# Optimization experiments

Hardware: AMD Instinct MI355X
Metric: run time of the kernel (lower is better)

## Reference

```python
import jax, jax.numpy as jnp
import numpy as np

VOCAB, EMB, HID = 50000, 1024, 2048
BATCH, SEQ = 256, 128


def _lstm_cell(x, h, c, W_ih, W_hh, b_ih, b_hh):
    # PyTorch LSTMCell: gates ordered (i, f, g, o), each of width HID
    gates = x @ W_ih.T + b_ih + h @ W_hh.T + b_hh  # [B, 4H]
    i, f, g, o = jnp.split(gates, 4, axis=-1)
    c_new = jax.nn.sigmoid(f) * c + jax.nn.sigmoid(i) * jnp.tanh(g)
    h_new = jax.nn.sigmoid(o) * jnp.tanh(c_new)
    return h_new, c_new


def setup_inputs() -> dict:
    key = jax.random.key(0)
    ks = jax.random.split(key, 11)
    s_e = 1.0 / np.sqrt(EMB)
    s_h = 1.0 / np.sqrt(HID)
    return {
        "inputs": jax.random.randint(ks[0], (BATCH, SEQ), 0, VOCAB, dtype=jnp.int64)
        if jax.config.jax_enable_x64 else jax.random.randint(ks[0], (BATCH, SEQ), 0, VOCAB, dtype=jnp.int32),
        "embed_table": jax.random.normal(ks[1], (VOCAB, EMB), jnp.float32),
        "W_ih_f": jax.random.normal(ks[2], (4 * HID, EMB), jnp.float32) * s_e,
        "W_hh_f": jax.random.normal(ks[3], (4 * HID, HID), jnp.float32) * s_h,
        "b_ih_f": jax.random.normal(ks[4], (4 * HID,), jnp.float32) * s_h,
        "b_hh_f": jax.random.normal(ks[5], (4 * HID,), jnp.float32) * s_h,
        "W_ih_b": jax.random.normal(ks[6], (4 * HID, EMB), jnp.float32) * s_e,
        "W_hh_b": jax.random.normal(ks[7], (4 * HID, HID), jnp.float32) * s_h,
        "b_ih_b": jax.random.normal(ks[8], (4 * HID,), jnp.float32) * s_h,
        "b_hh_b": jax.random.normal(ks[9], (4 * HID,), jnp.float32) * s_h,
    }


def reference(inputs, embed_table, W_ih_f, W_hh_f, b_ih_f, b_hh_f,
              W_ih_b, W_hh_b, b_ih_b, b_hh_b):
    # inputs[inputs > vocab_size] = 0
    idx = jnp.where(inputs > VOCAB, 0, inputs)
    embeds = embed_table[idx]  # [B, S, E]
    B = embeds.shape[0]
    zeros = jnp.zeros((B, HID), embeds.dtype)

    # Original forward loop feeds the (never-updated, all-zero) backward states
    # and discards cell state, so only the LAST timestep determines h_forward.
    h_fwd, _ = _lstm_cell(embeds[:, -1], zeros, zeros, W_ih_f, W_hh_f, b_ih_f, b_hh_f)

    # Backward loop: h recurses (t = S-1 .. 0), cell state stays zero (it is discarded).
    xs = jnp.flip(embeds, axis=1).transpose(1, 0, 2)  # [S, B, E], time-major reversed

    def step(h, x_t):
        h_new, _ = _lstm_cell(x_t, h, zeros, W_ih_b, W_hh_b, b_ih_b, b_hh_b)
        return h_new, None

    h_bwd, _ = jax.lax.scan(step, zeros, xs)

    return jnp.concatenate([h_fwd, h_bwd], axis=1)  # [B, 2H]
```

## Files before the change

kernel.cpp:

```cpp
#include <hip/hip_runtime.h>


#define B_    256
#define S_    128
#define E_    1024
#define H_    2048
#define VOC_  50000

typedef __bf16 bf16;
typedef bf16  bf16x8 __attribute__((ext_vector_type(8)));
typedef float f32x4  __attribute__((ext_vector_type(4)));
typedef float f32x16 __attribute__((ext_vector_type(16)));

typedef const char __attribute__((address_space(1)))* gas1_t;
typedef char       __attribute__((address_space(3)))* las3_t;

__global__ __launch_bounds__(256) void pack_w(const float* __restrict__ W,
                                              char* __restrict__ dst, int nchunks) {
  int p = blockIdx.x * 256 + threadIdx.x;
  int lane = p & 63; p >>= 6;
  int kk   = p & 3;  p >>= 2;
  int g    = p % 3;  p /= 3;
  int hl   = p & 1;  p >>= 1;
  int c    = p % nchunks;
  int jstrip = p / nchunks;
  int K  = nchunks * 64;
  int j  = jstrip * 32 + (lane & 31);
  int k0 = c * 64 + kk * 16 + (lane >> 5) * 8;
  int grow = j + (g == 1 ? 4096 : (g == 2 ? 6144 : 0));
  const float* src = W + (size_t)grow * K + k0;
  f32x4 v0 = *(const f32x4*)src;
  f32x4 v1 = *(const f32x4*)(src + 4);
  float f[8] = {v0[0], v0[1], v0[2], v0[3], v1[0], v1[1], v1[2], v1[3]};
  bf16x8 o;
#pragma unroll
  for (int e = 0; e < 8; ++e) {
    float x = f[e];
    bf16 hb = (bf16)x;
    o[e] = hl ? (bf16)(x - (float)hb) : hb;
  }
  size_t off = (size_t)(jstrip * nchunks + c) * 24576
             + (size_t)((hl * 3 + g) * 4 + kk) * 1024 + lane * 16;
  *(bf16x8*)(dst + off) = o;
}

__global__ __launch_bounds__(256) void pack_bias(const float* __restrict__ bib,
                                                 const float* __restrict__ bhb,
                                                 const float* __restrict__ bif,
                                                 const float* __restrict__ bhf,
                                                 float* __restrict__ B3B,
                                                 float* __restrict__ B3F) {
  int t = blockIdx.x * 256 + threadIdx.x;
  int which = t / 6144;
  int r = t % 6144;
  int g = r >> 11, j = r & 2047;
  int grow = j + (g == 1 ? 4096 : (g == 2 ? 6144 : 0));
  if (which == 0) B3B[g * 2048 + j] = bib[grow] + bhb[grow];
  else            B3F[g * 2048 + j] = bif[grow] + bhf[grow];
}

__global__ __launch_bounds__(256) void gather_k(const int* __restrict__ inputs,
                                                const float* __restrict__ emb,
                                                char* __restrict__ XH,
                                                char* __restrict__ XL) {
  int p = blockIdx.x * 256 + threadIdx.x;
  int l   = p & 63; p >>= 6;
  int k16 = p & 63; p >>= 6;
  int b32 = p & 7;  p >>= 3;
  int t   = p;
  int b  = b32 * 32 + (l & 31);
  int e0 = k16 * 16 + (l >> 5) * 8;
  int s  = (S_ - 1) - t;
  int iv = inputs[b * S_ + s];
  if ((unsigned)iv >= (unsigned)VOC_) iv = 0;
  const float* src = emb + (size_t)iv * E_ + e0;
  f32x4 v0 = *(const f32x4*)src;
  f32x4 v1 = *(const f32x4*)(src + 4);
  float f[8] = {v0[0], v0[1], v0[2], v0[3], v1[0], v1[1], v1[2], v1[3]};
  bf16x8 vh, vl;
#pragma unroll
  for (int e = 0; e < 8; ++e) {
    bf16 hb = (bf16)f[e];
    vh[e] = hb;
    vl[e] = (bf16)(f[e] - (float)hb);
  }
  size_t off = (size_t)t * 524288 + (size_t)(k16 * 8 + b32) * 1024 + l * 16;
  *(bf16x8*)(XH + off) = vh;
  *(bf16x8*)(XL + off) = vl;
}

__device__ __forceinline__ void gemm4(const char* __restrict__ aH,
                                      const char* __restrict__ aL,
                                      const char* __restrict__ wp,
                                      int kb16,
                                      float* __restrict__ dst,
                                      char* sm) {
  const int tid = threadIdx.x;
  const int wid = tid >> 6, lane = tid & 63;
  f32x16 acc[3] = {};

  auto stage = [&](int c, int buf) {
    const char* src = wp + (size_t)c * 24576;
#pragma unroll
    for (int i = 0; i < 3; ++i) {
      int off = (i * 8 + wid) * 1024;
      __builtin_amdgcn_global_load_lds((gas1_t)(src + off + lane * 16),
                                       (las3_t)(sm + buf * 24576 + off), 16, 0, 0);
    }
  };

  stage(0, 0);
  __syncthreads();
#pragma unroll
  for (int c = 0; c < 4; ++c) {
    if (c < 3) stage(c + 1, (c + 1) & 1);
    const char* bs = sm + (c & 1) * 24576;
#pragma unroll
    for (int kk = 0; kk < 4; ++kk) {
      const size_t aoff = (size_t)((kb16 + c * 4 + kk) * 8 + wid) * 1024 + lane * 16;
      bf16x8 AH = *(const bf16x8*)(aH + aoff);
      bf16x8 AL = *(const bf16x8*)(aL + aoff);
#pragma unroll
      for (int g = 0; g < 3; ++g) {
        bf16x8 BH = *(const bf16x8*)(bs + (size_t)(g * 4 + kk) * 1024 + lane * 16);
        bf16x8 BL = *(const bf16x8*)(bs + (size_t)((g + 3) * 4 + kk) * 1024 + lane * 16);
        acc[g] = __builtin_amdgcn_mfma_f32_32x32x16_bf16(AH, BH, acc[g], 0, 0, 0);
        acc[g] = __builtin_amdgcn_mfma_f32_32x32x16_bf16(AL, BH, acc[g], 0, 0, 0);
        acc[g] = __builtin_amdgcn_mfma_f32_32x32x16_bf16(AH, BL, acc[g], 0, 0, 0);
      }
    }
    __syncthreads();
  }
#pragma unroll
  for (int g = 0; g < 3; ++g)
#pragma unroll
    for (int r = 0; r < 16; ++r) {
      int row = (r & 3) + ((r >> 2) << 3) + ((lane >> 5) << 2);
      int b = wid * 32 + row;
      dst[(size_t)b * 96 + g * 32 + (lane & 31)] = acc[g][r];
    }
}

__global__ __launch_bounds__(512, 4) void step_gemm(
    const char* __restrict__ hH, const char* __restrict__ hL,
    const char* __restrict__ xH, const char* __restrict__ xL,
    const char* __restrict__ whh, const char* __restrict__ wihb,
    float* __restrict__ PR, float* __restrict__ XPslot) {
  __shared__ __attribute__((aligned(16))) char sm[49152];
  int bx = blockIdx.x;
  if (bx < 512) {
    int n = bx >> 3, s = bx & 7;
    gemm4(hH, hL, whh + (size_t)(n * 32 + s * 4) * 24576, s * 16,
          PR + (size_t)(s * 64 + n) * 24576, sm);
  } else {
    int i = bx - 512, n = i >> 2, s = i & 3;
    gemm4(xH, xL, wihb + (size_t)(n * 16 + s * 4) * 24576, s * 16,
          XPslot + (size_t)(s * 64 + n) * 24576, sm);
  }
}

__global__ __launch_bounds__(512, 4) void pre_gemm(
    const char* __restrict__ x0H, const char* __restrict__ x0L,
    const char* __restrict__ x1H, const char* __restrict__ x1L,
    const char* __restrict__ wihf, const char* __restrict__ wihb,
    float* __restrict__ FP, float* __restrict__ XP0, float* __restrict__ XP1) {
  __shared__ __attribute__((aligned(16))) char sm[49152];
  int bx = blockIdx.x;
  int grp = bx >> 8, i = bx & 255, n = i >> 2, s = i & 3;
  const char *aH, *aL, *wp; float* dst;
  if (grp == 0)      { aH = x0H; aL = x0L; wp = wihf; dst = FP;  }
  else if (grp == 1) { aH = x0H; aL = x0L; wp = wihb; dst = XP0; }
  else               { aH = x1H; aL = x1L; wp = wihb; dst = XP1; }
  gemm4(aH, aL, wp + (size_t)(n * 16 + s * 4) * 24576, s * 16,
        dst + (size_t)(s * 64 + n) * 24576, sm);
}

__device__ __forceinline__ float sig_(float x) {
  x = fminf(fmaxf(x, -30.f), 30.f);
  return 1.f / (1.f + __expf(-x));
}
__device__ __forceinline__ float tanh_(float x) {
  x = fminf(fmaxf(x, -15.f), 15.f);
  float e = __expf(2.f * x);
  return (e - 1.f) / (e + 1.f);
}

__global__ __launch_bounds__(256) void act_k(
    const float* __restrict__ PR, int nrs,
    const float* __restrict__ XPs, int nxs,
    const float* __restrict__ bias3,
    char* __restrict__ hH, char* __restrict__ hL,
    float* __restrict__ out, int outcol) {
  __shared__ float lds[32][33];
  const int n = blockIdx.x & 63, bo = blockIdx.x >> 6;
  const int tid = threadIdx.x;
  const int j = tid & 31, bs = tid >> 5;
  float ai[4], ag[4], ao[4];
  {
    float b0 = bias3[n * 32 + j];
    float b1 = bias3[2048 + n * 32 + j];
    float b2 = bias3[4096 + n * 32 + j];
#pragma unroll
    for (int r = 0; r < 4; ++r) { ai[r] = b0; ag[r] = b1; ao[r] = b2; }
  }
  for (int s = 0; s < nrs; ++s) {
    const float* p = PR + (size_t)(s * 64 + n) * 24576;
#pragma unroll
    for (int r = 0; r < 4; ++r) {
      int b = bo * 32 + r * 8 + bs;
      ai[r] += p[b * 96 + j];
      ag[r] += p[b * 96 + 32 + j];
      ao[r] += p[b * 96 + 64 + j];
    }
  }
  for (int s = 0; s < nxs; ++s) {
    const float* p = XPs + (size_t)(s * 64 + n) * 24576;
#pragma unroll
    for (int r = 0; r < 4; ++r) {
      int b = bo * 32 + r * 8 + bs;
      ai[r] += p[b * 96 + j];
      ag[r] += p[b * 96 + 32 + j];
      ao[r] += p[b * 96 + 64 + j];
    }
  }
  float hv[4];
#pragma unroll
  for (int r = 0; r < 4; ++r)
    hv[r] = sig_(ao[r]) * tanh_(sig_(ai[r]) * tanh_(ag[r]));

  if (out) {
#pragma unroll
    for (int r = 0; r < 4; ++r)
      out[(size_t)(bo * 32 + r * 8 + bs) * 4096 + outcol + n * 32 + j] = hv[r];
  }
  if (hH) {
#pragma unroll
    for (int r = 0; r < 4; ++r) lds[r * 8 + bs][j] = hv[r];
    __syncthreads();
    const int hl = tid >> 7, lx = tid & 127, joct = lx >> 5, bl = lx & 31;
    bf16x8 w;
#pragma unroll
    for (int e = 0; e < 8; ++e) {
      float v = lds[bl][joct * 8 + e];
      bf16 hb = (bf16)v;
      w[e] = hl ? (bf16)(v - (float)hb) : hb;
    }
    const int jg = n * 32 + joct * 8, bg = bo * 32 + bl;
    size_t off = (size_t)((jg >> 4) * 8 + (bg >> 5)) * 1024
               + (size_t)((bg & 31) + ((jg >> 3) & 1) * 32) * 16;
    *(bf16x8*)((hl ? hL : hH) + off) = w;
  }
}

extern "C" void kernel_launch(void* const* d_in, const int* in_sizes, int n_in,
                              void* d_out, int out_size, void* d_ws, size_t ws_size,
                              hipStream_t stream) {
  const int*   inputs = (const int*)d_in[0];
  const float* embed  = (const float*)d_in[1];
  const float* Wihf   = (const float*)d_in[2];
  const float* bihf   = (const float*)d_in[4];
  const float* bhhf   = (const float*)d_in[5];
  const float* Wihb   = (const float*)d_in[6];
  const float* Whhb   = (const float*)d_in[7];
  const float* bihb   = (const float*)d_in[8];
  const float* bhhb   = (const float*)d_in[9];
  float* out = (float*)d_out;
  char*  ws  = (char*)d_ws;

  size_t o = 0;
  char*  WHHp  = ws + o; o += 50331648;
  char*  WIHBp = ws + o; o += 25165824;
  char*  XRH   = ws + o; o += 67108864;
  char*  XRL   = ws + o; o += 67108864;
  float* XP    = (float*)(ws + o); o += 75497472;
  float* PR    = (float*)(ws + o); o += 50331648;
  char*  WIHFp = (char*)PR;
  char*  HB    = ws + o; o += 4194304;
  float* B3B   = (float*)(ws + o); o += 24576;
  float* B3F   = (float*)(ws + o); o += 24576;

  const size_t XPS = 25165824 / 4;
  float* FP = XP + 2 * XPS;

  hipMemsetAsync(HB, 0, 4194304, stream);

  pack_w<<<12288, 256, 0, stream>>>(Whhb, WHHp, 32);
  pack_w<<<6144, 256, 0, stream>>>(Wihb, WIHBp, 16);
  pack_w<<<6144, 256, 0, stream>>>(Wihf, WIHFp, 16);
  pack_bias<<<48, 256, 0, stream>>>(bihb, bhhb, bihf, bhhf, B3B, B3F);
  gather_k<<<16384, 256, 0, stream>>>(inputs, embed, XRH, XRL);

  pre_gemm<<<768, 512, 0, stream>>>(XRH, XRL, XRH + 524288, XRL + 524288,
                                    WIHFp, WIHBp, FP, XP, XP + XPS);
  act_k<<<512, 256, 0, stream>>>(FP, 0, FP, 4, B3F, nullptr, nullptr, out, 0);

  char* hHi[2] = {HB, HB + 2097152};
  char* hLo[2] = {HB + 1048576, HB + 3145728};

  for (int t = 0; t < S_; ++t) {
    int tx = (t + 2 > 127) ? 127 : t + 2;
    step_gemm<<<768, 512, 0, stream>>>(
        hHi[t & 1], hLo[t & 1],
        XRH + (size_t)tx * 524288, XRL + (size_t)tx * 524288,
        WHHp, WIHBp, PR, XP + (size_t)((t + 2) % 3) * XPS);
    act_k<<<512, 256, 0, stream>>>(
        PR, 8, XP + (size_t)(t % 3) * XPS, 4, B3B,
        (t < 127) ? hHi[(t & 1) ^ 1] : nullptr,
        (t < 127) ? hLo[(t & 1) ^ 1] : nullptr,
        (t == 127) ? out : nullptr, 2048);
  }
}
```

Baseline: 7.061 ms.

## Fuse recurrent GEMM, input projection and activation into one per-step kernel

Replaces the split-K step GEMM plus separate activation/reduction kernel with a single fused kernel. Each of 64 blocks walks the full K range (hidden plus input chunks) and applies the LSTM gate nonlinearities in registers. It writes the next hidden state directly in the packed bf16 hi/lo layout, and the bias layout is reordered to match. This removes the large fp32 partial-sum buffers and their write/read traffic, plus one launch per timestep. In exchange, only 64 blocks run per step with a long serial K loop, which leaves most CUs idle and lengthens per-block latency.

```diff
diff --git a/kernel.cpp b/kernel.cpp
--- a/kernel.cpp
+++ b/kernel.cpp
@@ -53,10 +53,10 @@
   int t = blockIdx.x * 256 + threadIdx.x;
   int which = t / 6144;
   int r = t % 6144;
-  int g = r >> 11, j = r & 2047;
-  int grow = j + (g == 1 ? 4096 : (g == 2 ? 6144 : 0));
-  if (which == 0) B3B[g * 2048 + j] = bib[grow] + bhb[grow];
-  else            B3F[g * 2048 + j] = bif[grow] + bhf[grow];
+  int n = r / 96, q = r % 96, g = q >> 5, j = q & 31;
+  int grow = n * 32 + j + (g == 1 ? 4096 : (g == 2 ? 6144 : 0));
+  if (which == 0) B3B[r] = bib[grow] + bhb[grow];
+  else            B3F[r] = bif[grow] + bhf[grow];
 }
 
 __global__ __launch_bounds__(256) void gather_k(const int* __restrict__ inputs,
@@ -89,18 +89,34 @@
   *(bf16x8*)(XL + off) = vl;
 }
 
-__device__ __forceinline__ void gemm4(const char* __restrict__ aH,
-                                      const char* __restrict__ aL,
-                                      const char* __restrict__ wp,
-                                      int kb16,
-                                      float* __restrict__ dst,
-                                      char* sm) {
+__device__ __forceinline__ float sig_(float x) {
+  x = fminf(fmaxf(x, -30.f), 30.f);
+  return 1.f / (1.f + __expf(-x));
+}
+__device__ __forceinline__ float tanh_(float x) {
+  x = fminf(fmaxf(x, -15.f), 15.f);
+  float e = __expf(2.f * x);
+  return (e - 1.f) / (e + 1.f);
+}
+
+__global__ __launch_bounds__(512, 1) void fused_step(
+    const char* __restrict__ hH, const char* __restrict__ hL, int nHc,
+    const char* __restrict__ xH, const char* __restrict__ xL, int nXc,
+    const char* __restrict__ Wh, const char* __restrict__ Wx,
+    const float* __restrict__ bias3,
+    char* __restrict__ hOutH, char* __restrict__ hOutL,
+    float* __restrict__ out, int outcol) {
+  __shared__ __attribute__((aligned(16))) char sm[49152];
+  const int n = blockIdx.x;
   const int tid = threadIdx.x;
   const int wid = tid >> 6, lane = tid & 63;
+  const int nc = nHc + nXc;
+
   f32x16 acc[3] = {};
 
   auto stage = [&](int c, int buf) {
-    const char* src = wp + (size_t)c * 24576;
+    const char* src = (c < nHc) ? (Wh + (size_t)(n * nHc + c) * 24576)
+                                : (Wx + (size_t)(n * nXc + (c - nHc)) * 24576);
 #pragma unroll
     for (int i = 0; i < 3; ++i) {
       int off = (i * 8 + wid) * 1024;
@@ -109,15 +125,15 @@
     }
   };
 
-  stage(0, 0);
-  __syncthreads();
-#pragma unroll
-  for (int c = 0; c < 4; ++c) {
-    if (c < 3) stage(c + 1, (c + 1) & 1);
-    const char* bs = sm + (c & 1) * 24576;
+  auto compute = [&](int c, int buf) {
+    const char *aH, *aL;
+    int kb;
+    if (c < nHc) { aH = hH; aL = hL; kb = c * 4; }
+    else         { aH = xH; aL = xL; kb = (c - nHc) * 4; }
+    const char* bs = sm + buf * 24576;
 #pragma unroll
     for (int kk = 0; kk < 4; ++kk) {
-      const size_t aoff = (size_t)((kb16 + c * 4 + kk) * 8 + wid) * 1024 + lane * 16;
+      const size_t aoff = (size_t)((kb + kk) * 8 + wid) * 1024 + lane * 16;
       bf16x8 AH = *(const bf16x8*)(aH + aoff);
       bf16x8 AL = *(const bf16x8*)(aL + aoff);
 #pragma unroll
@@ -129,126 +145,58 @@
         acc[g] = __builtin_amdgcn_mfma_f32_32x32x16_bf16(AH, BL, acc[g], 0, 0, 0);
       }
     }
+  };
+
+  stage(0, 0);
+  __syncthreads();
+  for (int c = 0; c < nc; ++c) {
+    if (c + 1 < nc) stage(c + 1, (c + 1) & 1);
+    compute(c, c & 1);
     __syncthreads();
   }
-#pragma unroll
-  for (int g = 0; g < 3; ++g)
+
+  const int j = lane & 31;
+  const float bi = bias3[n * 96 + j];
+  const float bg = bias3[n * 96 + 32 + j];
+  const float bo = bias3[n * 96 + 64 + j];
+  float hv[16];
+#pragma unroll
+  for (int r = 0; r < 16; ++r)
+    hv[r] = sig_(acc[2][r] + bo) * tanh_(sig_(acc[0][r] + bi) * tanh_(acc[1][r] + bg));
+
+  if (out) {
 #pragma unroll
     for (int r = 0; r < 16; ++r) {
       int row = (r & 3) + ((r >> 2) << 3) + ((lane >> 5) << 2);
-      int b = wid * 32 + row;
-      dst[(size_t)b * 96 + g * 32 + (lane & 31)] = acc[g][r];
-    }
-}
-
-__global__ __launch_bounds__(512, 4) void step_gemm(
-    const char* __restrict__ hH, const char* __restrict__ hL,
-    const char* __restrict__ xH, const char* __restrict__ xL,
-    const char* __restrict__ whh, const char* __restrict__ wihb,
-    float* __restrict__ PR, float* __restrict__ XPslot) {
-  __shared__ __attribute__((aligned(16))) char sm[49152];
-  int bx = blockIdx.x;
-  if (bx < 512) {
-    int n = bx >> 3, s = bx & 7;
-    gemm4(hH, hL, whh + (size_t)(n * 32 + s * 4) * 24576, s * 16,
-          PR + (size_t)(s * 64 + n) * 24576, sm);
-  } else {
-    int i = bx - 512, n = i >> 2, s = i & 3;
-    gemm4(xH, xL, wihb + (size_t)(n * 16 + s * 4) * 24576, s * 16,
-          XPslot + (size_t)(s * 64 + n) * 24576, sm);
-  }
-}
-
-__global__ __launch_bounds__(512, 4) void pre_gemm(
-    const char* __restrict__ x0H, const char* __restrict__ x0L,
-    const char* __restrict__ x1H, const char* __restrict__ x1L,
-    const char* __restrict__ wihf, const char* __restrict__ wihb,
-    float* __restrict__ FP, float* __restrict__ XP0, float* __restrict__ XP1) {
-  __shared__ __attribute__((aligned(16))) char sm[49152];
-  int bx = blockIdx.x;
-  int grp = bx >> 8, i = bx & 255, n = i >> 2, s = i & 3;
-  const char *aH, *aL, *wp; float* dst;
-  if (grp == 0)      { aH = x0H; aL = x0L; wp = wihf; dst = FP;  }
-  else if (grp == 1) { aH = x0H; aL = x0L; wp = wihb; dst = XP0; }
-  else               { aH = x1H; aL = x1L; wp = wihb; dst = XP1; }
-  gemm4(aH, aL, wp + (size_t)(n * 16 + s * 4) * 24576, s * 16,
-        dst + (size_t)(s * 64 + n) * 24576, sm);
-}
-
-__device__ __forceinline__ float sig_(float x) {
-  x = fminf(fmaxf(x, -30.f), 30.f);
-  return 1.f / (1.f + __expf(-x));
-}
-__device__ __forceinline__ float tanh_(float x) {
-  x = fminf(fmaxf(x, -15.f), 15.f);
-  float e = __expf(2.f * x);
-  return (e - 1.f) / (e + 1.f);
-}
-
-__global__ __launch_bounds__(256) void act_k(
-    const float* __restrict__ PR, int nrs,
-    const float* __restrict__ XPs, int nxs,
-    const float* __restrict__ bias3,
-    char* __restrict__ hH, char* __restrict__ hL,
-    float* __restrict__ out, int outcol) {
-  __shared__ float lds[32][33];
-  const int n = blockIdx.x & 63, bo = blockIdx.x >> 6;
-  const int tid = threadIdx.x;
-  const int j = tid & 31, bs = tid >> 5;
-  float ai[4], ag[4], ao[4];
-  {
-    float b0 = bias3[n * 32 + j];
-    float b1 = bias3[2048 + n * 32 + j];
-    float b2 = bias3[4096 + n * 32 + j];
-#pragma unroll
-    for (int r = 0; r < 4; ++r) { ai[r] = b0; ag[r] = b1; ao[r] = b2; }
-  }
-  for (int s = 0; s < nrs; ++s) {
-    const float* p = PR + (size_t)(s * 64 + n) * 24576;
-#pragma unroll
-    for (int r = 0; r < 4; ++r) {
-      int b = bo * 32 + r * 8 + bs;
-      ai[r] += p[b * 96 + j];
-      ag[r] += p[b * 96 + 32 + j];
-      ao[r] += p[b * 96 + 64 + j];
-    }
-  }
-  for (int s = 0; s < nxs; ++s) {
-    const float* p = XPs + (size_t)(s * 64 + n) * 24576;
-#pragma unroll
-    for (int r = 0; r < 4; ++r) {
-      int b = bo * 32 + r * 8 + bs;
-      ai[r] += p[b * 96 + j];
-      ag[r] += p[b * 96 + 32 + j];
-      ao[r] += p[b * 96 + 64 + j];
-    }
-  }
-  float hv[4];
-#pragma unroll
-  for (int r = 0; r < 4; ++r)
-    hv[r] = sig_(ao[r]) * tanh_(sig_(ai[r]) * tanh_(ag[r]));
-
-  if (out) {
-#pragma unroll
-    for (int r = 0; r < 4; ++r)
-      out[(size_t)(bo * 32 + r * 8 + bs) * 4096 + outcol + n * 32 + j] = hv[r];
-  }
-  if (hH) {
-#pragma unroll
-    for (int r = 0; r < 4; ++r) lds[r * 8 + bs][j] = hv[r];
+      out[(size_t)(wid * 32 + row) * 4096 + outcol + n * 32 + j] = hv[r];
+    }
+  }
+
+  if (hOutH) {
+    float* tp = (float*)sm + (size_t)wid * 1152;
+#pragma unroll
+    for (int r = 0; r < 16; ++r) {
+      int row = (r & 3) + ((r >> 2) << 3) + ((lane >> 5) << 2);
+      tp[row * 36 + j] = hv[r];
+    }
     __syncthreads();
-    const int hl = tid >> 7, lx = tid & 127, joct = lx >> 5, bl = lx & 31;
-    bf16x8 w;
-#pragma unroll
-    for (int e = 0; e < 8; ++e) {
-      float v = lds[bl][joct * 8 + e];
-      bf16 hb = (bf16)v;
-      w[e] = hl ? (bf16)(v - (float)hb) : hb;
-    }
-    const int jg = n * 32 + joct * 8, bg = bo * 32 + bl;
-    size_t off = (size_t)((jg >> 4) * 8 + (bg >> 5)) * 1024
-               + (size_t)((bg & 31) + ((jg >> 3) & 1) * 32) * 16;
-    *(bf16x8*)((hl ? hL : hH) + off) = w;
+#pragma unroll
+    for (int s = 0; s < 2; ++s) {
+      const float* rp = tp + (lane & 31) * 36 + s * 16 + (lane >> 5) * 8;
+      f32x4 v0 = *(const f32x4*)rp;
+      f32x4 v1 = *(const f32x4*)(rp + 4);
+      float f[8] = {v0[0], v0[1], v0[2], v0[3], v1[0], v1[1], v1[2], v1[3]};
+      bf16x8 vh, vl;
+#pragma unroll
+      for (int e = 0; e < 8; ++e) {
+        bf16 hb = (bf16)f[e];
+        vh[e] = hb;
+        vl[e] = (bf16)(f[e] - (float)hb);
+      }
+      size_t off = (size_t)((n * 2 + s) * 8 + wid) * 1024 + lane * 16;
+      *(bf16x8*)(hOutH + off) = vh;
+      *(bf16x8*)(hOutL + off) = vl;
+    }
   }
 }
 
@@ -270,17 +218,12 @@
   size_t o = 0;
   char*  WHHp  = ws + o; o += 50331648;
   char*  WIHBp = ws + o; o += 25165824;
+  char*  WIHFp = ws + o; o += 25165824;
   char*  XRH   = ws + o; o += 67108864;
   char*  XRL   = ws + o; o += 67108864;
-  float* XP    = (float*)(ws + o); o += 75497472;
-  float* PR    = (float*)(ws + o); o += 50331648;
-  char*  WIHFp = (char*)PR;
   char*  HB    = ws + o; o += 4194304;
   float* B3B   = (float*)(ws + o); o += 24576;
   float* B3F   = (float*)(ws + o); o += 24576;
-
-  const size_t XPS = 25165824 / 4;
-  float* FP = XP + 2 * XPS;
 
   hipMemsetAsync(HB, 0, 4194304, stream);
 
@@ -290,23 +233,21 @@
   pack_bias<<<48, 256, 0, stream>>>(bihb, bhhb, bihf, bhhf, B3B, B3F);
   gather_k<<<16384, 256, 0, stream>>>(inputs, embed, XRH, XRL);
 
-  pre_gemm<<<768, 512, 0, stream>>>(XRH, XRL, XRH + 524288, XRL + 524288,
-                                    WIHFp, WIHBp, FP, XP, XP + XPS);
-  act_k<<<512, 256, 0, stream>>>(FP, 0, FP, 4, B3F, nullptr, nullptr, out, 0);
+  fused_step<<<64, 512, 0, stream>>>(nullptr, nullptr, 0, XRH, XRL, 16,
+                                     nullptr, WIHFp, B3F,
+                                     nullptr, nullptr, out, 0);
 
   char* hHi[2] = {HB, HB + 2097152};
   char* hLo[2] = {HB + 1048576, HB + 3145728};
 
   for (int t = 0; t < S_; ++t) {
-    int tx = (t + 2 > 127) ? 127 : t + 2;
-    step_gemm<<<768, 512, 0, stream>>>(
-        hHi[t & 1], hLo[t & 1],
-        XRH + (size_t)tx * 524288, XRL + (size_t)tx * 524288,
-        WHHp, WIHBp, PR, XP + (size_t)((t + 2) % 3) * XPS);
-    act_k<<<512, 256, 0, stream>>>(
-        PR, 8, XP + (size_t)(t % 3) * XPS, 4, B3B,
-        (t < 127) ? hHi[(t & 1) ^ 1] : nullptr,
-        (t < 127) ? hLo[(t & 1) ^ 1] : nullptr,
-        (t == 127) ? out : nullptr, 2048);
-  }
-}
+    bool last = (t == S_ - 1);
+    fused_step<<<64, 512, 0, stream>>>(
+        hHi[t & 1], hLo[t & 1], 32,
+        XRH + (size_t)t * 524288, XRL + (size_t)t * 524288, 16,
+        WHHp, WIHBp, B3B,
+        last ? nullptr : hHi[(t & 1) ^ 1],
+        last ? nullptr : hLo[(t & 1) ^ 1],
+        last ? out : nullptr, 2048);
+  }
+}
```

After: 16.06 ms. +127.5%, slower.
